# Optimization experiments

Hardware: AMD Instinct MI355X
Metric: run time of the kernel (lower is better)

## Reference

```python
import jax, jax.numpy as jnp
import numpy as np

EPS_LN = 1e-3
EPS_ATTN = 1e-8
D = 256       # slot_dim == feature_dim (required by the torch code)
H_MLP = 512
NUM_ITERS = 3  # step == 0 -> num_initial_iterations
SCALE = D ** (-0.5)


def _layernorm(x, g, b):
    m = jnp.mean(x, axis=-1, keepdims=True)
    v = jnp.mean(jnp.square(x - m), axis=-1, keepdims=True)
    return (x - m) * jax.lax.rsqrt(v + EPS_LN) * g + b


def _gru_cell(x, h, W_ih, b_ih, W_hh, b_hh):
    # torch GRUCell: W_ih [3D, D], W_hh [3D, D], gate order r, z, n
    gi = x @ W_ih.T + b_ih
    gh = h @ W_hh.T + b_hh
    i_r, i_z, i_n = jnp.split(gi, 3, axis=-1)
    h_r, h_z, h_n = jnp.split(gh, 3, axis=-1)
    r = jax.nn.sigmoid(i_r + h_r)
    z = jax.nn.sigmoid(i_z + h_z)
    n = jnp.tanh(i_n + r * h_n)
    return (1.0 - z) * n + z * h


def setup_inputs() -> dict:
    key = jax.random.key(0)
    ks = jax.random.split(key, 16)
    s = 0.02
    inp = {
        "inputs": jax.random.normal(ks[0], (32, 4096, D), jnp.float32),
        "slots": jax.random.normal(ks[1], (32, 8, D), jnp.float32),
        "step": 0,
        "ln_in_g": jnp.ones((D,), jnp.float32),
        "ln_in_b": jnp.zeros((D,), jnp.float32),
        "ln_slot_g": jnp.ones((D,), jnp.float32),
        "ln_slot_b": jnp.zeros((D,), jnp.float32),
        "ln_mlp_g": jnp.ones((D,), jnp.float32),
        "ln_mlp_b": jnp.zeros((D,), jnp.float32),
        "Wq": jax.random.normal(ks[2], (D, D), jnp.float32) * s,
        "bq": jnp.zeros((D,), jnp.float32),
        "Wk": jax.random.normal(ks[3], (D, D), jnp.float32) * s,
        "bk": jnp.zeros((D,), jnp.float32),
        "Wv": jax.random.normal(ks[4], (D, D), jnp.float32) * s,
        "bv": jnp.zeros((D,), jnp.float32),
        "W_ih": jax.random.normal(ks[5], (3 * D, D), jnp.float32) * s,
        "b_ih": jnp.zeros((3 * D,), jnp.float32),
        "W_hh": jax.random.normal(ks[6], (3 * D, D), jnp.float32) * s,
        "b_hh": jnp.zeros((3 * D,), jnp.float32),
        "W1": jax.random.normal(ks[7], (H_MLP, D), jnp.float32) * s,
        "b1": jnp.zeros((H_MLP,), jnp.float32),
        "W2": jax.random.normal(ks[8], (D, H_MLP), jnp.float32) * s,
        "b2": jnp.zeros((D,), jnp.float32),
    }
    return inp


def reference(inputs, slots, step, ln_in_g, ln_in_b, ln_slot_g, ln_slot_b,
              ln_mlp_g, ln_mlp_b, Wq, bq, Wk, bk, Wv, bv,
              W_ih, b_ih, W_hh, b_hh, W1, b1, W2, b2):
    B = inputs.shape[0]
    x = _layernorm(inputs, ln_in_g, ln_in_b)          # [B, N, D]
    k = x @ Wk.T + bk                                  # [B, N, D]
    v = x @ Wv.T + bv                                  # [B, N, D]
    num_iters = NUM_ITERS  # step == 0 -> num_initial_iterations
    for _ in range(num_iters):
        slots_prev = slots
        s_n = _layernorm(slots, ln_slot_g, ln_slot_b)  # [B, S, D]
        q = s_n @ Wq.T + bq                            # [B, S, D]
        dots = jnp.einsum('bid,bjd->bij', q, k) * SCALE  # [B, S, N]
        attn = jax.nn.softmax(dots, axis=1) + EPS_ATTN   # competitive over slots
        attn = attn / jnp.sum(attn, axis=-1, keepdims=True)
        updates = jnp.einsum('bij,bjd->bid', attn, v)  # [B, S, D]
        slots = _gru_cell(updates.reshape(-1, D), slots_prev.reshape(-1, D),
                          W_ih, b_ih, W_hh, b_hh).reshape(B, -1, D)
        mlp = jax.nn.relu(_layernorm(slots, ln_mlp_g, ln_mlp_b) @ W1.T + b1) @ W2.T + b2
        slots = slots + mlp
    return slots
```

## Files before the change

kernel.cpp:

```cpp
#include <hip/hip_runtime.h>
#include <stdint.h>


typedef __attribute__((ext_vector_type(8))) short bf16x8;
typedef __attribute__((ext_vector_type(4))) float f32x4;

__device__ __forceinline__ float bf2f_lo(uint32_t u) {
    union { uint32_t u; float f; } v; v.u = u << 16; return v.f;
}
__device__ __forceinline__ float bf2f_hi(uint32_t u) {
    union { uint32_t u; float f; } v; v.u = u & 0xffff0000u; return v.f;
}
__device__ __forceinline__ unsigned short f2bf(float f) {
    union { float f; uint32_t u; } v; v.f = f;
    return (unsigned short)((v.u + 0x7fffu + ((v.u >> 16) & 1u)) >> 16);
}
__device__ __forceinline__ void unpack8(uint4 v, float* f) {
    f[0] = bf2f_lo(v.x); f[1] = bf2f_hi(v.x); f[2] = bf2f_lo(v.y); f[3] = bf2f_hi(v.y);
    f[4] = bf2f_lo(v.z); f[5] = bf2f_hi(v.z); f[6] = bf2f_lo(v.w); f[7] = bf2f_hi(v.w);
}
__device__ __forceinline__ float sigf(float x) { return 1.0f / (1.0f + __expf(-x)); }
__device__ __forceinline__ void gld_lds16(const void* g, void* l) {
    __builtin_amdgcn_global_load_lds(
        (__attribute__((address_space(1))) unsigned int*)g,
        (__attribute__((address_space(3))) unsigned int*)l, 16, 0, 0);
}

__global__ __launch_bounds__(256) void prep_k(
    const float* __restrict__ in, const float* __restrict__ ln_in_g,
    const float* __restrict__ ln_in_b, unsigned short* __restrict__ xbf,
    const float* __restrict__ Wk, const float* __restrict__ Wv,
    const float* __restrict__ W_ih, const float* __restrict__ W_hh,
    const float* __restrict__ W1, const float* __restrict__ W2,
    const float* __restrict__ bk, const float* __restrict__ bv,
    const float* __restrict__ b_ih, const float* __restrict__ b_hh,
    unsigned short* __restrict__ Wkv, unsigned short* __restrict__ Wg,
    unsigned short* __restrict__ W1b, unsigned short* __restrict__ W2b,
    float* __restrict__ bkv, float* __restrict__ bg,
    const float* __restrict__ slots_in, const float* __restrict__ g_slot,
    const float* __restrict__ b_slot, const float* __restrict__ Wq,
    const float* __restrict__ bq, unsigned short* __restrict__ qbuf,
    float* __restrict__ upd) {
    __shared__ __align__(16) unsigned short A1[8 * 264];
    int bid = blockIdx.x, t = threadIdx.x;
    int wave = t >> 6, lane = t & 63;

    if (bid < 8192) {
        size_t rb = (size_t)bid * 16 + wave * 4;
        const float* rp = in + rb * 256 + lane * 4;
        float4 x0 = *(const float4*)(rp);
        float4 x1 = *(const float4*)(rp + 256);
        float4 x2 = *(const float4*)(rp + 512);
        float4 x3 = *(const float4*)(rp + 768);
        float s0 = x0.x + x0.y + x0.z + x0.w, q0 = x0.x*x0.x + x0.y*x0.y + x0.z*x0.z + x0.w*x0.w;
        float s1 = x1.x + x1.y + x1.z + x1.w, q1 = x1.x*x1.x + x1.y*x1.y + x1.z*x1.z + x1.w*x1.w;
        float s2 = x2.x + x2.y + x2.z + x2.w, q2 = x2.x*x2.x + x2.y*x2.y + x2.z*x2.z + x2.w*x2.w;
        float s3 = x3.x + x3.y + x3.z + x3.w, q3 = x3.x*x3.x + x3.y*x3.y + x3.z*x3.z + x3.w*x3.w;
#pragma unroll
        for (int off = 32; off > 0; off >>= 1) {
            s0 += __shfl_xor(s0, off, 64);  q0 += __shfl_xor(q0, off, 64);
            s1 += __shfl_xor(s1, off, 64);  q1 += __shfl_xor(q1, off, 64);
            s2 += __shfl_xor(s2, off, 64);  q2 += __shfl_xor(q2, off, 64);
            s3 += __shfl_xor(s3, off, 64);  q3 += __shfl_xor(q3, off, 64);
        }
        float4 g4 = *(const float4*)(ln_in_g + lane * 4);
        float4 b4 = *(const float4*)(ln_in_b + lane * 4);
        float4 xs[4] = {x0, x1, x2, x3};
        float ss[4] = {s0, s1, s2, s3}, qq[4] = {q0, q1, q2, q3};
#pragma unroll
        for (int i = 0; i < 4; ++i) {
            float mean = ss[i] * (1.0f / 256.0f);
            float rstd = rsqrtf(qq[i] * (1.0f / 256.0f) - mean * mean + 1e-3f);
            float4 x = xs[i];
            uint2 o;
            o.x = (uint32_t)f2bf((x.x - mean) * rstd * g4.x + b4.x) |
                  ((uint32_t)f2bf((x.y - mean) * rstd * g4.y + b4.y) << 16);
            o.y = (uint32_t)f2bf((x.z - mean) * rstd * g4.z + b4.z) |
                  ((uint32_t)f2bf((x.w - mean) * rstd * g4.w + b4.w) << 16);
            size_t row = rb + i;
            int dst = (((lane >> 1) ^ ((int)row & 7)) << 3) + (lane & 1) * 4;
            *(uint2*)(xbf + row * 256 + dst) = o;
        }
        return;
    }
    if (bid < 11520) {
        int i = (bid - 8192) * 256 + t;
        if (i < 131072) {
            float v = (i < 65536) ? Wk[i] : Wv[i - 65536];
            int col = i >> 8, k = i & 255;
            int dk = ((((k >> 3) ^ (col & 7)) << 3) | (k & 7));
            Wkv[col * 256 + dk] = f2bf(v);
        } else if (i < 524288) {
            int j = i - 131072;
            Wg[j] = f2bf(j < 196608 ? W_ih[j] : W_hh[j - 196608]);
        } else if (i < 655360) W1b[i - 524288] = f2bf(W1[i - 524288]);
        else                   W2b[i - 655360] = f2bf(W2[i - 655360]);
        if (i < 512)           bkv[i] = (i < 256 ? bk[i] : bv[i - 256]);
        else if (i < 2048)   { int j = i - 512; bg[j] = (j < 768 ? b_ih[j] : b_hh[j - 768]); }
        return;
    }
    if (bid >= 11552) {
        int i = (bid - 11552) * 1024 + t * 4;
        if (i < 65792) *(float4*)(upd + i) = make_float4(0.f, 0.f, 0.f, 0.f);
        return;
    }
    int b = bid - 11520;
    {
        float4 g4 = *(const float4*)(g_slot + lane * 4);
        float4 b4 = *(const float4*)(b_slot + lane * 4);
#pragma unroll
        for (int rep = 0; rep < 2; ++rep) {
            int s = wave * 2 + rep;
            float4 x = *(const float4*)(slots_in + (size_t)b * 2048 + s * 256 + lane * 4);
            float sm = x.x + x.y + x.z + x.w;
            float sq = x.x * x.x + x.y * x.y + x.z * x.z + x.w * x.w;
#pragma unroll
            for (int off = 32; off > 0; off >>= 1) {
                sm += __shfl_xor(sm, off, 64);
                sq += __shfl_xor(sq, off, 64);
            }
            float mean = sm * (1.0f / 256.0f);
            float rstd = rsqrtf(sq * (1.0f / 256.0f) - mean * mean + 1e-3f);
            uint2 o;
            o.x = (uint32_t)f2bf((x.x - mean) * rstd * g4.x + b4.x) |
                  ((uint32_t)f2bf((x.y - mean) * rstd * g4.y + b4.y) << 16);
            o.y = (uint32_t)f2bf((x.z - mean) * rstd * g4.z + b4.z) |
                  ((uint32_t)f2bf((x.w - mean) * rstd * g4.w + b4.w) << 16);
            *(uint2*)&A1[s * 264 + lane * 4] = o;
        }
    }
    __syncthreads();
    {
        bf16x8 af[8];
#pragma unroll
        for (int ks = 0; ks < 8; ++ks)
            af[ks] = *(const bf16x8*)&A1[(lane & 15) * 264 + ks * 32 + (lane >> 4) * 8];
#pragma unroll
        for (int nt = 0; nt < 4; ++nt) {
            int n0 = (wave * 4 + nt) * 16;
            f32x4 a = {0.f, 0.f, 0.f, 0.f};
#pragma unroll
            for (int ks = 0; ks < 8; ++ks) {
                const float* wp = Wq + (size_t)(n0 + (lane & 15)) * 256 +
                                  ks * 32 + (lane >> 4) * 8;
                float4 wa = *(const float4*)wp;
                float4 wb = *(const float4*)(wp + 4);
                bf16x8 bfr;
                bfr[0] = (short)f2bf(wa.x); bfr[1] = (short)f2bf(wa.y);
                bfr[2] = (short)f2bf(wa.z); bfr[3] = (short)f2bf(wa.w);
                bfr[4] = (short)f2bf(wb.x); bfr[5] = (short)f2bf(wb.y);
                bfr[6] = (short)f2bf(wb.z); bfr[7] = (short)f2bf(wb.w);
                a = __builtin_amdgcn_mfma_f32_16x16x32_bf16(af[ks], bfr, a, 0, 0, 0);
            }
            int col = n0 + (lane & 15);
            float bs = bq[col];
#pragma unroll
            for (int r = 0; r < 4; ++r) {
                int row = (lane >> 4) * 4 + r;
                if (row < 8)
                    qbuf[((size_t)b * 8 + row) * 256 + col] = f2bf(a[r] + bs);
            }
        }
    }
}

__global__ __launch_bounds__(256) void gemm_kv(const unsigned short* __restrict__ X,
                                               const unsigned short* __restrict__ W,
                                               const float* __restrict__ bkv,
                                               unsigned short* __restrict__ Ko,
                                               unsigned short* __restrict__ Vo) {
    __shared__ __align__(16) unsigned short As[128 * 64];
    __shared__ __align__(16) unsigned short Bs[128 * 64];
    int t = threadIdx.x, wave = t >> 6, lane = t & 63;
    int wr = wave >> 1, wc = wave & 1;
    int bid = blockIdx.x;
    int m0 = (((bid >> 5) << 3) | (bid & 7)) * 128;
    int j0 = ((bid >> 3) & 3) * 128;

    f32x4 acc[4][4];
#pragma unroll
    for (int i = 0; i < 4; ++i)
#pragma unroll
        for (int j = 0; j < 4; ++j)
#pragma unroll
            for (int r = 0; r < 4; ++r) acc[i][j][r] = 0.f;

    for (int kb = 0; kb < 4; ++kb) {
        int k0 = kb * 64;
#pragma unroll
        for (int i = 0; i < 4; ++i) {
            int rbase = wave * 32 + i * 8;
            gld_lds16(X + (size_t)(m0 + rbase + (lane >> 3)) * 256 + k0 + (lane & 7) * 8,
                      &As[rbase * 64]);
            gld_lds16(W + (size_t)(j0 + rbase + (lane >> 3)) * 256 + k0 + (lane & 7) * 8,
                      &Bs[rbase * 64]);
        }
        __syncthreads();
#pragma unroll
        for (int kk = 0; kk < 64; kk += 32) {
            int koff = kk + (lane >> 4) * 8;
            int cl = koff >> 3;
            bf16x8 af[4], bf[4];
#pragma unroll
            for (int ti = 0; ti < 4; ++ti) {
                int r = wr * 64 + ti * 16 + (lane & 15);
                af[ti] = *(const bf16x8*)&As[r * 64 + ((cl ^ (r & 7)) << 3)];
            }
#pragma unroll
            for (int tj = 0; tj < 4; ++tj) {
                int c = wc * 64 + tj * 16 + (lane & 15);
                bf[tj] = *(const bf16x8*)&Bs[c * 64 + ((cl ^ (c & 7)) << 3)];
            }
#pragma unroll
            for (int ti = 0; ti < 4; ++ti)
#pragma unroll
                for (int tj = 0; tj < 4; ++tj)
                    acc[ti][tj] = __builtin_amdgcn_mfma_f32_16x16x32_bf16(
                        af[ti], bf[tj], acc[ti][tj], 0, 0, 0);
        }
        __syncthreads();
    }
    bool isK = (j0 < 256);
    unsigned short* base = isK ? Ko : Vo;
#pragma unroll
    for (int ti = 0; ti < 4; ++ti)
#pragma unroll
        for (int tj = 0; tj < 4; ++tj) {
            int col = j0 + wc * 64 + tj * 16 + (lane & 15);
            float bias = bkv[col];
            int outc = col & 255;
#pragma unroll
            for (int r = 0; r < 4; ++r) {
                int row = m0 + wr * 64 + ti * 16 + (lane >> 4) * 4 + r;
                base[(size_t)row * 256 + outc] = f2bf(acc[ti][tj][r] + bias);
            }
        }
}

__global__ __launch_bounds__(256) void attn_fused(
    const unsigned short* __restrict__ qb, const unsigned short* __restrict__ K,
    const unsigned short* __restrict__ V,
    float* __restrict__ upd, float* __restrict__ sums) {
    __shared__ __align__(16) unsigned short qs[8 * 256];
    __shared__ __align__(16) float atf[8 * 256];
    __shared__ __align__(16) float pr[4][8 * 256];
    __shared__ float ssum[8];
    int b = blockIdx.x, ch = blockIdx.y, t = threadIdx.x;
    int wave = t >> 6, lane = t & 63;

    *(uint4*)&qs[t * 8] = ((const uint4*)(qb + b * 2048))[t];
    if (t < 8) ssum[t] = 0.f;
    __syncthreads();

    int sg = t >> 7, np = t & 127;
    int nbase = ch * 256 + np * 2;
    const unsigned short* kr = K + ((size_t)b * 4096 + nbase) * 256;
    float acc[4][2];
#pragma unroll
    for (int i = 0; i < 4; ++i) { acc[i][0] = 0.f; acc[i][1] = 0.f; }
    for (int c = 0; c < 32; ++c) {
        float qf[4][8];
#pragma unroll
        for (int si = 0; si < 4; ++si)
            unpack8(*(const uint4*)&qs[(sg * 4 + si) * 256 + c * 8], qf[si]);
#pragma unroll
        for (int r = 0; r < 2; ++r) {
            float kf[8];
            unpack8(*(const uint4*)(kr + (size_t)r * 256 + c * 8), kf);
#pragma unroll
            for (int si = 0; si < 4; ++si)
                acc[si][r] += qf[si][0] * kf[0] + qf[si][1] * kf[1] +
                              qf[si][2] * kf[2] + qf[si][3] * kf[3] +
                              qf[si][4] * kf[4] + qf[si][5] * kf[5] +
                              qf[si][6] * kf[6] + qf[si][7] * kf[7];
        }
    }
#pragma unroll
    for (int si = 0; si < 4; ++si) {
        atf[(sg * 4 + si) * 256 + np * 2 + 0] = acc[si][0] * 0.0625f;
        atf[(sg * 4 + si) * 256 + np * 2 + 1] = acc[si][1] * 0.0625f;
    }
    __syncthreads();

    {
        int n = t;
        float v[8];
#pragma unroll
        for (int s = 0; s < 8; ++s) v[s] = atf[s * 256 + n];
        float m = v[0];
#pragma unroll
        for (int s = 1; s < 8; ++s) m = fmaxf(m, v[s]);
        float sum = 0.f;
#pragma unroll
        for (int s = 0; s < 8; ++s) { v[s] = __expf(v[s] - m); sum += v[s]; }
        float inv = 1.0f / sum;
        float ts[8];
#pragma unroll
        for (int s = 0; s < 8; ++s) {
            float a = v[s] * inv + 1e-8f;
            atf[s * 256 + n] = a;
            ts[s] = a;
        }
#pragma unroll
        for (int s = 0; s < 8; ++s) {
#pragma unroll
            for (int off = 32; off > 0; off >>= 1)
                ts[s] += __shfl_xor(ts[s], off, 64);
        }
        if (lane == 0) {
#pragma unroll
            for (int s = 0; s < 8; ++s) atomicAdd(&ssum[s], ts[s]);
        }
    }
    __syncthreads();
    if (t < 8) atomicAdd(&sums[b * 8 + t], ssum[t]);

    float ua[8][4];
#pragma unroll
    for (int s = 0; s < 8; ++s)
#pragma unroll
        for (int k = 0; k < 4; ++k) ua[s][k] = 0.f;
    const unsigned short* vb = V + ((size_t)b * 4096 + ch * 256 + wave * 64) * 256 + lane * 4;
    for (int g = 0; g < 16; ++g) {
        int nl = wave * 64 + g * 4;
        float4 a4[8];
#pragma unroll
        for (int s = 0; s < 8; ++s) a4[s] = *(const float4*)&atf[s * 256 + nl];
        const unsigned short* vrow = vb + (size_t)g * 4 * 256;
#define UPD_STEP(kk, comp)                                                     \
        {                                                                      \
            uint2 vv = *(const uint2*)(vrow + (size_t)kk * 256);               \
            float v0 = bf2f_lo(vv.x), v1 = bf2f_hi(vv.x);                      \
            float v2 = bf2f_lo(vv.y), v3 = bf2f_hi(vv.y);                      \
            _Pragma("unroll")                                                  \
            for (int s = 0; s < 8; ++s) {                                      \
                float a = a4[s].comp;                                          \
                ua[s][0] += a * v0; ua[s][1] += a * v1;                        \
                ua[s][2] += a * v2; ua[s][3] += a * v3;                        \
            }                                                                  \
        }
        UPD_STEP(0, x) UPD_STEP(1, y) UPD_STEP(2, z) UPD_STEP(3, w)
#undef UPD_STEP
    }
#pragma unroll
    for (int s = 0; s < 8; ++s)
        *(float4*)&pr[wave][s * 256 + lane * 4] = *(float4*)ua[s];
    __syncthreads();
    for (int i = t; i < 2048; i += 256) {
        float vsum = pr[0][i] + pr[1][i] + pr[2][i] + pr[3][i];
        atomicAdd(&upd[(size_t)b * 2048 + i], vsum);
    }
}

__global__ __launch_bounds__(512, 1) void slot_tail(
    const float* __restrict__ upd, const float* __restrict__ sums,
    float* __restrict__ upd_w, float* __restrict__ sums_w,
    const float* __restrict__ cur,
    const unsigned short* __restrict__ Wg, const float* __restrict__ bg,
    const float* __restrict__ g_mlp, const float* __restrict__ b_mlp,
    const unsigned short* __restrict__ W1b, const float* __restrict__ b1,
    const unsigned short* __restrict__ W2b, const float* __restrict__ b2,
    const float* __restrict__ g_slot, const float* __restrict__ b_slot,
    const unsigned short* __restrict__ Wqb, const float* __restrict__ bq,
    float* __restrict__ slots_out, unsigned short* __restrict__ qbuf,
    int do_q) {
    __shared__ float gts[8 * 1536];
    __shared__ float hn[2048];
    __shared__ float sn[2048];
    __shared__ __align__(16) unsigned short A1u[8 * 264];
    __shared__ __align__(16) unsigned short A1h[8 * 264];
    __shared__ __align__(16) unsigned short A1[8 * 264];
    __shared__ __align__(16) unsigned short A2[8 * 520];
    __shared__ float ssum8[8];
    int b = blockIdx.x, t = threadIdx.x;
    int wave = t >> 6, lane = t & 63;

    if (t < 8) ssum8[t] = sums[b * 8 + t];
    __syncthreads();
    for (int idx = t; idx < 2048; idx += 512) {
        int row = idx >> 8, d = idx & 255;
        A1u[row * 264 + d] = f2bf(upd[(size_t)b * 2048 + idx] / ssum8[row]);
        A1h[row * 264 + d] = f2bf(cur[(size_t)b * 2048 + idx]);
    }
    __syncthreads();
    for (int idx = t; idx < 2048; idx += 512) upd_w[(size_t)b * 2048 + idx] = 0.f;
    if (t < 8) sums_w[b * 8 + t] = 0.f;

    {
        const unsigned short* Af = (wave < 4) ? A1u : A1h;
        bf16x8 af[8];
#pragma unroll
        for (int ks = 0; ks < 8; ++ks)
            af[ks] = *(const bf16x8*)&Af[(lane & 15) * 264 + ks * 32 + (lane >> 4) * 8];
#pragma unroll
        for (int nt = 0; nt < 12; ++nt) {
            int n0 = wave * 192 + nt * 16;
            f32x4 a = {0.f, 0.f, 0.f, 0.f};
#pragma unroll
            for (int ks = 0; ks < 8; ++ks) {
                bf16x8 bfr = *(const bf16x8*)(Wg + (size_t)(n0 + (lane & 15)) * 256 +
                                              ks * 32 + (lane >> 4) * 8);
                a = __builtin_amdgcn_mfma_f32_16x16x32_bf16(af[ks], bfr, a, 0, 0, 0);
            }
            int col = n0 + (lane & 15);
            float bs = bg[col];
#pragma unroll
            for (int r = 0; r < 4; ++r) {
                int row = (lane >> 4) * 4 + r;
                if (row < 8) gts[row * 1536 + col] = a[r] + bs;
            }
        }
    }
    __syncthreads();

#pragma unroll
    for (int p = 0; p < 4; ++p) {
        int idx = p * 512 + t;
        int s = idx >> 8, j = idx & 255;
        const float* gr = &gts[s * 1536];
        float r  = sigf(gr[j] + gr[768 + j]);
        float z  = sigf(gr[256 + j] + gr[1024 + j]);
        float nn = tanhf(gr[512 + j] + r * gr[1280 + j]);
        float h  = cur[(size_t)b * 2048 + idx];
        hn[idx] = (1.0f - z) * nn + z * h;
    }
    __syncthreads();

    {
        float4 g4 = *(const float4*)(g_mlp + lane * 4);
        float4 b4 = *(const float4*)(b_mlp + lane * 4);
        int s = wave;
        float4 x = *(const float4*)&hn[s * 256 + lane * 4];
        float sm = x.x + x.y + x.z + x.w;
        float sq = x.x * x.x + x.y * x.y + x.z * x.z + x.w * x.w;
#pragma unroll
        for (int off = 32; off > 0; off >>= 1) {
            sm += __shfl_xor(sm, off, 64);
            sq += __shfl_xor(sq, off, 64);
        }
        float mean = sm * (1.0f / 256.0f);
        float rstd = rsqrtf(sq * (1.0f / 256.0f) - mean * mean + 1e-3f);
        uint2 o;
        o.x = (uint32_t)f2bf((x.x - mean) * rstd * g4.x + b4.x) |
              ((uint32_t)f2bf((x.y - mean) * rstd * g4.y + b4.y) << 16);
        o.y = (uint32_t)f2bf((x.z - mean) * rstd * g4.z + b4.z) |
              ((uint32_t)f2bf((x.w - mean) * rstd * g4.w + b4.w) << 16);
        *(uint2*)&A1[s * 264 + lane * 4] = o;
    }
    __syncthreads();

    {
        bf16x8 af[8];
#pragma unroll
        for (int ks = 0; ks < 8; ++ks)
            af[ks] = *(const bf16x8*)&A1[(lane & 15) * 264 + ks * 32 + (lane >> 4) * 8];
#pragma unroll
        for (int nt = 0; nt < 4; ++nt) {
            int n0 = (wave * 4 + nt) * 16;
            f32x4 a = {0.f, 0.f, 0.f, 0.f};
#pragma unroll
            for (int ks = 0; ks < 8; ++ks) {
                bf16x8 bfr = *(const bf16x8*)(W1b + (size_t)(n0 + (lane & 15)) * 256 +
                                              ks * 32 + (lane >> 4) * 8);
                a = __builtin_amdgcn_mfma_f32_16x16x32_bf16(af[ks], bfr, a, 0, 0, 0);
            }
            int col = n0 + (lane & 15);
            float bs = b1[col];
#pragma unroll
            for (int r = 0; r < 4; ++r) {
                int row = (lane >> 4) * 4 + r;
                if (row < 8) A2[row * 520 + col] = f2bf(fmaxf(a[r] + bs, 0.f));
            }
        }
    }
    __syncthreads();

    {
        bf16x8 af[16];
#pragma unroll
        for (int ks = 0; ks < 16; ++ks)
            af[ks] = *(const bf16x8*)&A2[(lane & 15) * 520 + ks * 32 + (lane >> 4) * 8];
#pragma unroll
        for (int nt = 0; nt < 2; ++nt) {
            int n0 = (wave * 2 + nt) * 16;
            f32x4 a = {0.f, 0.f, 0.f, 0.f};
#pragma unroll
            for (int ks = 0; ks < 16; ++ks) {
                bf16x8 bfr = *(const bf16x8*)(W2b + (size_t)(n0 + (lane & 15)) * 512 +
                                              ks * 32 + (lane >> 4) * 8);
                a = __builtin_amdgcn_mfma_f32_16x16x32_bf16(af[ks], bfr, a, 0, 0, 0);
            }
            int col = n0 + (lane & 15);
            float bs = b2[col];
#pragma unroll
            for (int r = 0; r < 4; ++r) {
                int row = (lane >> 4) * 4 + r;
                if (row < 8) {
                    float v = a[r] + bs + hn[row * 256 + col];
                    sn[row * 256 + col] = v;
                    slots_out[((size_t)b * 8 + row) * 256 + col] = v;
                }
            }
        }
    }
    if (!do_q) return;
    __syncthreads();

    {
        float4 g4 = *(const float4*)(g_slot + lane * 4);
        float4 b4 = *(const float4*)(b_slot + lane * 4);
        int s = wave;
        float4 x = *(const float4*)&sn[s * 256 + lane * 4];
        float sm = x.x + x.y + x.z + x.w;
        float sq = x.x * x.x + x.y * x.y + x.z * x.z + x.w * x.w;
#pragma unroll
        for (int off = 32; off > 0; off >>= 1) {
            sm += __shfl_xor(sm, off, 64);
            sq += __shfl_xor(sq, off, 64);
        }
        float mean = sm * (1.0f / 256.0f);
        float rstd = rsqrtf(sq * (1.0f / 256.0f) - mean * mean + 1e-3f);
        uint2 o;
        o.x = (uint32_t)f2bf((x.x - mean) * rstd * g4.x + b4.x) |
              ((uint32_t)f2bf((x.y - mean) * rstd * g4.y + b4.y) << 16);
        o.y = (uint32_t)f2bf((x.z - mean) * rstd * g4.z + b4.z) |
              ((uint32_t)f2bf((x.w - mean) * rstd * g4.w + b4.w) << 16);
        *(uint2*)&A1[s * 264 + lane * 4] = o;
    }
    __syncthreads();

    {
        bf16x8 af[8];
#pragma unroll
        for (int ks = 0; ks < 8; ++ks)
            af[ks] = *(const bf16x8*)&A1[(lane & 15) * 264 + ks * 32 + (lane >> 4) * 8];
#pragma unroll
        for (int nt = 0; nt < 2; ++nt) {
            int n0 = (wave * 2 + nt) * 16;
            f32x4 a = {0.f, 0.f, 0.f, 0.f};
#pragma unroll
            for (int ks = 0; ks < 8; ++ks) {
                bf16x8 bfr = *(const bf16x8*)(Wqb + (size_t)(n0 + (lane & 15)) * 256 +
                                              ks * 32 + (lane >> 4) * 8);
                a = __builtin_amdgcn_mfma_f32_16x16x32_bf16(af[ks], bfr, a, 0, 0, 0);
            }
            int col = n0 + (lane & 15);
            float bs = bq[col];
#pragma unroll
            for (int r = 0; r < 4; ++r) {
                int row = (lane >> 4) * 4 + r;
                if (row < 8)
                    qbuf[((size_t)b * 8 + row) * 256 + col] = f2bf(a[r] + bs);
            }
        }
    }
}

extern "C" void kernel_launch(void* const* d_in, const int* in_sizes, int n_in,
                              void* d_out, int out_size, void* d_ws, size_t ws_size,
                              hipStream_t stream) {
    const float* inputs    = (const float*)d_in[0];
    const float* slots_in  = (const float*)d_in[1];
    const float* ln_in_g   = (const float*)d_in[3];
    const float* ln_in_b   = (const float*)d_in[4];
    const float* ln_slot_g = (const float*)d_in[5];
    const float* ln_slot_b = (const float*)d_in[6];
    const float* ln_mlp_g  = (const float*)d_in[7];
    const float* ln_mlp_b  = (const float*)d_in[8];
    const float* Wq   = (const float*)d_in[9];
    const float* bq   = (const float*)d_in[10];
    const float* Wk   = (const float*)d_in[11];
    const float* bk   = (const float*)d_in[12];
    const float* Wv   = (const float*)d_in[13];
    const float* bv   = (const float*)d_in[14];
    const float* W_ih = (const float*)d_in[15];
    const float* b_ih = (const float*)d_in[16];
    const float* W_hh = (const float*)d_in[17];
    const float* b_hh = (const float*)d_in[18];
    const float* W1   = (const float*)d_in[19];
    const float* b1   = (const float*)d_in[20];
    const float* W2   = (const float*)d_in[21];
    const float* b2   = (const float*)d_in[22];

    char* p = (char*)d_ws;
    size_t off = 0;
    auto take = [&](size_t bytes) -> char* {
        char* r = p + off;
        off += (bytes + 255) & ~(size_t)255;
        return r;
    };
    unsigned short* xbf  = (unsigned short*)take((size_t)131072 * 256 * 2);
    unsigned short* Kb   = (unsigned short*)take((size_t)131072 * 256 * 2);
    unsigned short* Vb   = (unsigned short*)take((size_t)131072 * 256 * 2);
    unsigned short* Wkv  = (unsigned short*)take(131072 * 2);
    unsigned short* Wg   = (unsigned short*)take(393216 * 2);
    unsigned short* W1b  = (unsigned short*)take(131072 * 2);
    unsigned short* W2b  = (unsigned short*)take(131072 * 2);
    unsigned short* Wqb  = (unsigned short*)take(65536 * 2);
    float* bkv   = (float*)take(512 * 4);
    float* bg    = (float*)take(1536 * 4);
    unsigned short* qbuf = (unsigned short*)take(65536 * 2);
    float* upd   = (float*)take((65536 + 256) * 4);
    float* sums  = upd + 65536;
    float* sA    = (float*)take(65536 * 4);
    float* sB    = (float*)take(65536 * 4);

    prep_k<<<11617, 256, 0, stream>>>(inputs, ln_in_g, ln_in_b, xbf,
                                      Wk, Wv, W_ih, W_hh, W1, W2,
                                      bk, bv, b_ih, b_hh,
                                      Wkv, Wg, W1b, W2b, bkv, bg,
                                      slots_in, ln_slot_g, ln_slot_b, Wq, bq, qbuf,
                                      upd);
    {
        struct L { static __global__ void k(const float* __restrict__ Wq,
                                            unsigned short* __restrict__ Wqb) {
            int i = blockIdx.x * 256 + threadIdx.x;
            Wqb[i] = f2bf(Wq[i]);
        } };
        L::k<<<256, 256, 0, stream>>>(Wq, Wqb);
    }
    gemm_kv<<<4096, 256, 0, stream>>>(xbf, Wkv, bkv, Kb, Vb);

    const float* cur = slots_in;
    float* nxt[3] = {sA, sB, (float*)d_out};
    for (int it = 0; it < 3; ++it) {
        attn_fused<<<dim3(32, 16), 256, 0, stream>>>(qbuf, Kb, Vb, upd, sums);
        slot_tail<<<32, 512, 0, stream>>>(upd, sums, upd, sums, cur, Wg, bg,
                                          ln_mlp_g, ln_mlp_b, W1b, b1, W2b, b2,
                                          ln_slot_g, ln_slot_b, Wqb, bq,
                                          nxt[it], qbuf, it < 2 ? 1 : 0);
        cur = nxt[it];
    }
    (void)in_sizes; (void)n_in; (void)out_size; (void)ws_size;
}
```

Baseline: 563.9 us.

## Use MFMA for attention dots, prefetch V rows, process 8 LN rows per wave

The attention kernel's q·k dot products move from scalar FMA loops to bf16 MFMA 16x16x32 instructions. The q tile in LDS is padded to 264 columns to avoid bank conflicts. The V accumulation loop now software-prefetches the next group of V rows into registers. Separately, the input layernorm handles 8 rows per wave instead of 4, which halves the block count of the prep kernel and raises memory-level parallelism, at the cost of more registers per thread.

```diff
diff --git a/kernel.cpp b/kernel.cpp
--- a/kernel.cpp
+++ b/kernel.cpp
@@ -45,46 +45,46 @@
     int bid = blockIdx.x, t = threadIdx.x;
     int wave = t >> 6, lane = t & 63;
 
-    if (bid < 8192) {
-        size_t rb = (size_t)bid * 16 + wave * 4;
+    if (bid < 4096) {
+        size_t rb = (size_t)bid * 32 + wave * 8;
         const float* rp = in + rb * 256 + lane * 4;
-        float4 x0 = *(const float4*)(rp);
-        float4 x1 = *(const float4*)(rp + 256);
-        float4 x2 = *(const float4*)(rp + 512);
-        float4 x3 = *(const float4*)(rp + 768);
-        float s0 = x0.x + x0.y + x0.z + x0.w, q0 = x0.x*x0.x + x0.y*x0.y + x0.z*x0.z + x0.w*x0.w;
-        float s1 = x1.x + x1.y + x1.z + x1.w, q1 = x1.x*x1.x + x1.y*x1.y + x1.z*x1.z + x1.w*x1.w;
-        float s2 = x2.x + x2.y + x2.z + x2.w, q2 = x2.x*x2.x + x2.y*x2.y + x2.z*x2.z + x2.w*x2.w;
-        float s3 = x3.x + x3.y + x3.z + x3.w, q3 = x3.x*x3.x + x3.y*x3.y + x3.z*x3.z + x3.w*x3.w;
+        float4 x[8];
+#pragma unroll
+        for (int i = 0; i < 8; ++i) x[i] = *(const float4*)(rp + i * 256);
+        float ss[8], qq[8];
+#pragma unroll
+        for (int i = 0; i < 8; ++i) {
+            ss[i] = x[i].x + x[i].y + x[i].z + x[i].w;
+            qq[i] = x[i].x * x[i].x + x[i].y * x[i].y + x[i].z * x[i].z + x[i].w * x[i].w;
+        }
 #pragma unroll
         for (int off = 32; off > 0; off >>= 1) {
-            s0 += __shfl_xor(s0, off, 64);  q0 += __shfl_xor(q0, off, 64);
-            s1 += __shfl_xor(s1, off, 64);  q1 += __shfl_xor(q1, off, 64);
-            s2 += __shfl_xor(s2, off, 64);  q2 += __shfl_xor(q2, off, 64);
-            s3 += __shfl_xor(s3, off, 64);  q3 += __shfl_xor(q3, off, 64);
+#pragma unroll
+            for (int i = 0; i < 8; ++i) {
+                ss[i] += __shfl_xor(ss[i], off, 64);
+                qq[i] += __shfl_xor(qq[i], off, 64);
+            }
         }
         float4 g4 = *(const float4*)(ln_in_g + lane * 4);
         float4 b4 = *(const float4*)(ln_in_b + lane * 4);
-        float4 xs[4] = {x0, x1, x2, x3};
-        float ss[4] = {s0, s1, s2, s3}, qq[4] = {q0, q1, q2, q3};
-#pragma unroll
-        for (int i = 0; i < 4; ++i) {
+#pragma unroll
+        for (int i = 0; i < 8; ++i) {
             float mean = ss[i] * (1.0f / 256.0f);
             float rstd = rsqrtf(qq[i] * (1.0f / 256.0f) - mean * mean + 1e-3f);
-            float4 x = xs[i];
+            float4 xx = x[i];
             uint2 o;
-            o.x = (uint32_t)f2bf((x.x - mean) * rstd * g4.x + b4.x) |
-                  ((uint32_t)f2bf((x.y - mean) * rstd * g4.y + b4.y) << 16);
-            o.y = (uint32_t)f2bf((x.z - mean) * rstd * g4.z + b4.z) |
-                  ((uint32_t)f2bf((x.w - mean) * rstd * g4.w + b4.w) << 16);
+            o.x = (uint32_t)f2bf((xx.x - mean) * rstd * g4.x + b4.x) |
+                  ((uint32_t)f2bf((xx.y - mean) * rstd * g4.y + b4.y) << 16);
+            o.y = (uint32_t)f2bf((xx.z - mean) * rstd * g4.z + b4.z) |
+                  ((uint32_t)f2bf((xx.w - mean) * rstd * g4.w + b4.w) << 16);
             size_t row = rb + i;
             int dst = (((lane >> 1) ^ ((int)row & 7)) << 3) + (lane & 1) * 4;
             *(uint2*)(xbf + row * 256 + dst) = o;
         }
         return;
     }
-    if (bid < 11520) {
-        int i = (bid - 8192) * 256 + t;
+    if (bid < 7168) {
+        int i = (bid - 4096) * 256 + t;
         if (i < 131072) {
             float v = (i < 65536) ? Wk[i] : Wv[i - 65536];
             int col = i >> 8, k = i & 255;
@@ -99,12 +99,12 @@
         else if (i < 2048)   { int j = i - 512; bg[j] = (j < 768 ? b_ih[j] : b_hh[j - 768]); }
         return;
     }
-    if (bid >= 11552) {
-        int i = (bid - 11552) * 1024 + t * 4;
+    if (bid >= 7200) {
+        int i = (bid - 7200) * 1024 + t * 4;
         if (i < 65792) *(float4*)(upd + i) = make_float4(0.f, 0.f, 0.f, 0.f);
         return;
     }
-    int b = bid - 11520;
+    int b = bid - 7168;
     {
         float4 g4 = *(const float4*)(g_slot + lane * 4);
         float4 b4 = *(const float4*)(b_slot + lane * 4);
@@ -241,44 +241,41 @@
     const unsigned short* __restrict__ qb, const unsigned short* __restrict__ K,
     const unsigned short* __restrict__ V,
     float* __restrict__ upd, float* __restrict__ sums) {
-    __shared__ __align__(16) unsigned short qs[8 * 256];
+    __shared__ __align__(16) unsigned short qs[8 * 264];
     __shared__ __align__(16) float atf[8 * 256];
     __shared__ __align__(16) float pr[4][8 * 256];
     __shared__ float ssum[8];
     int b = blockIdx.x, ch = blockIdx.y, t = threadIdx.x;
     int wave = t >> 6, lane = t & 63;
 
-    *(uint4*)&qs[t * 8] = ((const uint4*)(qb + b * 2048))[t];
+    *(uint4*)&qs[(t >> 5) * 264 + (t & 31) * 8] = ((const uint4*)(qb + (size_t)b * 2048))[t];
     if (t < 8) ssum[t] = 0.f;
     __syncthreads();
 
-    int sg = t >> 7, np = t & 127;
-    int nbase = ch * 256 + np * 2;
-    const unsigned short* kr = K + ((size_t)b * 4096 + nbase) * 256;
-    float acc[4][2];
-#pragma unroll
-    for (int i = 0; i < 4; ++i) { acc[i][0] = 0.f; acc[i][1] = 0.f; }
-    for (int c = 0; c < 32; ++c) {
-        float qf[4][8];
-#pragma unroll
-        for (int si = 0; si < 4; ++si)
-            unpack8(*(const uint4*)&qs[(sg * 4 + si) * 256 + c * 8], qf[si]);
-#pragma unroll
-        for (int r = 0; r < 2; ++r) {
-            float kf[8];
-            unpack8(*(const uint4*)(kr + (size_t)r * 256 + c * 8), kf);
-#pragma unroll
-            for (int si = 0; si < 4; ++si)
-                acc[si][r] += qf[si][0] * kf[0] + qf[si][1] * kf[1] +
-                              qf[si][2] * kf[2] + qf[si][3] * kf[3] +
-                              qf[si][4] * kf[4] + qf[si][5] * kf[5] +
-                              qf[si][6] * kf[6] + qf[si][7] * kf[7];
-        }
-    }
-#pragma unroll
-    for (int si = 0; si < 4; ++si) {
-        atf[(sg * 4 + si) * 256 + np * 2 + 0] = acc[si][0] * 0.0625f;
-        atf[(sg * 4 + si) * 256 + np * 2 + 1] = acc[si][1] * 0.0625f;
+    {
+        bf16x8 af[8];
+#pragma unroll
+        for (int ks = 0; ks < 8; ++ks)
+            af[ks] = *(const bf16x8*)&qs[(lane & 7) * 264 + ks * 32 + (lane >> 4) * 8];
+        const unsigned short* kb_ = K + ((size_t)b * 4096 + ch * 256) * 256;
+#pragma unroll
+        for (int nt = 0; nt < 4; ++nt) {
+            int n0 = (wave * 4 + nt) * 16;
+            const unsigned short* kp = kb_ + (size_t)(n0 + (lane & 15)) * 256 + (lane >> 4) * 8;
+            f32x4 a = {0.f, 0.f, 0.f, 0.f};
+#pragma unroll
+            for (int ks = 0; ks < 8; ++ks) {
+                bf16x8 bfr = *(const bf16x8*)(kp + ks * 32);
+                a = __builtin_amdgcn_mfma_f32_16x16x32_bf16(af[ks], bfr, a, 0, 0, 0);
+            }
+            if (lane < 32) {
+                int n = n0 + (lane & 15);
+                int s0 = (lane >> 4) * 4;
+#pragma unroll
+                for (int r = 0; r < 4; ++r)
+                    atf[(s0 + r) * 256 + n] = a[r] * 0.0625f;
+            }
+        }
     }
     __syncthreads();
 
@@ -321,17 +318,23 @@
 #pragma unroll
         for (int k = 0; k < 4; ++k) ua[s][k] = 0.f;
     const unsigned short* vb = V + ((size_t)b * 4096 + ch * 256 + wave * 64) * 256 + lane * 4;
+    uint2 vv[4], vn[4];
+#pragma unroll
+    for (int kk = 0; kk < 4; ++kk) vv[kk] = *(const uint2*)(vb + (size_t)kk * 256);
     for (int g = 0; g < 16; ++g) {
+        if (g < 15) {
+            const unsigned short* nrow = vb + (size_t)(g + 1) * 1024;
+#pragma unroll
+            for (int kk = 0; kk < 4; ++kk) vn[kk] = *(const uint2*)(nrow + (size_t)kk * 256);
+        }
         int nl = wave * 64 + g * 4;
         float4 a4[8];
 #pragma unroll
         for (int s = 0; s < 8; ++s) a4[s] = *(const float4*)&atf[s * 256 + nl];
-        const unsigned short* vrow = vb + (size_t)g * 4 * 256;
 #define UPD_STEP(kk, comp)                                                     \
         {                                                                      \
-            uint2 vv = *(const uint2*)(vrow + (size_t)kk * 256);               \
-            float v0 = bf2f_lo(vv.x), v1 = bf2f_hi(vv.x);                      \
-            float v2 = bf2f_lo(vv.y), v3 = bf2f_hi(vv.y);                      \
+            float v0 = bf2f_lo(vv[kk].x), v1 = bf2f_hi(vv[kk].x);              \
+            float v2 = bf2f_lo(vv[kk].y), v3 = bf2f_hi(vv[kk].y);              \
             _Pragma("unroll")                                                  \
             for (int s = 0; s < 8; ++s) {                                      \
                 float a = a4[s].comp;                                          \
@@ -341,6 +344,8 @@
         }
         UPD_STEP(0, x) UPD_STEP(1, y) UPD_STEP(2, z) UPD_STEP(3, w)
 #undef UPD_STEP
+#pragma unroll
+        for (int kk = 0; kk < 4; ++kk) vv[kk] = vn[kk];
     }
 #pragma unroll
     for (int s = 0; s < 8; ++s)
@@ -605,12 +610,12 @@
     float* sA    = (float*)take(65536 * 4);
     float* sB    = (float*)take(65536 * 4);
 
-    prep_k<<<11617, 256, 0, stream>>>(inputs, ln_in_g, ln_in_b, xbf,
-                                      Wk, Wv, W_ih, W_hh, W1, W2,
-                                      bk, bv, b_ih, b_hh,
-                                      Wkv, Wg, W1b, W2b, bkv, bg,
-                                      slots_in, ln_slot_g, ln_slot_b, Wq, bq, qbuf,
-                                      upd);
+    prep_k<<<7265, 256, 0, stream>>>(inputs, ln_in_g, ln_in_b, xbf,
+                                     Wk, Wv, W_ih, W_hh, W1, W2,
+                                     bk, bv, b_ih, b_hh,
+                                     Wkv, Wg, W1b, W2b, bkv, bg,
+                                     slots_in, ln_slot_g, ln_slot_b, Wq, bq, qbuf,
+                                     upd);
     {
         struct L { static __global__ void k(const float* __restrict__ Wq,
                                             unsigned short* __restrict__ Wqb) {
```

After: 522.4 us. 7.4% less time.
